# Kernel optimization log

Measured on AMD Instinct MI355X. Metric: run time of the kernel, lower is better.

## Reference

```python
import jax, jax.numpy as jnp
import numpy as np

CH = 256
HEADS = 4
RED = 8  # SE reduction on 2*CH channels


def _conv2d(x, w, pad):
    # x: [b,c,h,w], w: [o,i,kh,kw]
    return jax.lax.conv_general_dilated(
        x, w, window_strides=(1, 1), padding=[(pad, pad), (pad, pad)],
        dimension_numbers=('NCHW', 'OIHW', 'NCHW'))


def setup_inputs() -> dict:
    key = jax.random.key(0)
    ks = jax.random.split(key, 12)
    b, c, h, w = 4, CH, 64, 64
    c2 = 2 * c
    s = 0.02
    inp = {
        'color_feat': jax.random.normal(ks[0], (b, c, h, w), jnp.float32),
        'gray_feat': jax.random.normal(ks[1], (b, c, h, w), jnp.float32),
        'Wq': jax.random.normal(ks[2], (c, c), jnp.float32) * s,
        'Wk': jax.random.normal(ks[3], (c, c), jnp.float32) * s,
        'Wv': jax.random.normal(ks[4], (c, c), jnp.float32) * s,
        'Wproj': jax.random.normal(ks[5], (c, c), jnp.float32) * s,
        'ca_w1': jax.random.normal(ks[6], (c2 // RED, c2), jnp.float32) * s,
        'ca_w2': jax.random.normal(ks[7], (c2, c2 // RED), jnp.float32) * s,
        'sa_w': jax.random.normal(ks[8], (1, 2, 7, 7), jnp.float32) * s,
        'fuse_w': jax.random.normal(ks[9], (c, c2, 3, 3), jnp.float32) * s,
        'bn_gamma': jnp.ones((c,), jnp.float32),
        'bn_beta': jnp.zeros((c,), jnp.float32),
        'bn_mean': jnp.zeros((c,), jnp.float32),
        'bn_var': jnp.ones((c,), jnp.float32),
    }
    return inp


def reference(color_feat, gray_feat, Wq, Wk, Wv, Wproj, ca_w1, ca_w2,
              sa_w, fuse_w, bn_gamma, bn_beta, bn_mean, bn_var):
    b, c, h, w = color_feat.shape
    nh = HEADS
    d = c // nh
    scale = d ** -0.5

    def heads(x, W):
        # 1x1 conv then split heads: [b,c,h,w] -> [b,nh,hw,d]
        y = jnp.einsum('bchw,oc->bohw', x, W)
        return y.reshape(b, nh, d, h * w).transpose(0, 1, 3, 2)

    q = heads(color_feat, Wq)
    k = heads(gray_feat, Wk)
    v = heads(gray_feat, Wv)

    attn = jax.nn.softmax(jnp.einsum('bnid,bnjd->bnij', q, k) * scale, axis=-1)
    out = jnp.einsum('bnij,bnjd->bnid', attn, v)
    out = out.transpose(0, 1, 3, 2).reshape(b, c, h, w)
    out = jnp.einsum('bchw,oc->bohw', out, Wproj)

    cat = jnp.concatenate([out, gray_feat], axis=1)  # [b,2c,h,w]

    # Channel attention (SE with shared MLP on avg- and max-pooled vectors)
    def mlp(z):
        return jax.nn.relu(z @ ca_w1.T) @ ca_w2.T
    avg = cat.mean(axis=(2, 3))
    mx = cat.max(axis=(2, 3))
    wch = jax.nn.sigmoid(mlp(avg) + mlp(mx))[:, :, None, None]
    cat = cat * wch

    # Spatial attention: channel-mean/max -> 7x7 conv -> sigmoid gate
    sa_in = jnp.stack([cat.mean(axis=1), cat.max(axis=1)], axis=1)  # [b,2,h,w]
    wsp = jax.nn.sigmoid(_conv2d(sa_in, sa_w, pad=3))
    cat = cat * wsp

    # Fuse: 3x3 conv -> BatchNorm (inference stats) -> LeakyReLU(0.2)
    y = _conv2d(cat, fuse_w, pad=1)
    inv = bn_gamma / jnp.sqrt(bn_var + 1e-5)
    y = (y - bn_mean[None, :, None, None]) * inv[None, :, None, None] + bn_beta[None, :, None, None]
    return jnp.where(y > 0, y, 0.2 * y)
```

## Files before the change

kernel.cpp:

```cpp
#include <hip/hip_runtime.h>
#include <hip/hip_bf16.h>
#include <stdint.h>

#define HW_ 4096

typedef short bf16x8 __attribute__((ext_vector_type(8)));
typedef short short4v __attribute__((ext_vector_type(4)));
typedef short short8v __attribute__((ext_vector_type(8)));
typedef float f32x4 __attribute__((ext_vector_type(4)));
typedef float f32x16 __attribute__((ext_vector_type(16)));
typedef uint32_t u32x4 __attribute__((ext_vector_type(4)));

__device__ inline unsigned short f2bf(float x) {
  uint32_t u = __builtin_bit_cast(uint32_t, x);
  uint32_t r = ((u >> 16) & 1u) + 0x7fffu;
  return (unsigned short)((u + r) >> 16);
}
__device__ inline uint32_t cvt_pk_bf16(float lo, float hi) {
  uint32_t r;
  asm("v_cvt_pk_bf16_f32 %0, %1, %2" : "=v"(r) : "v"(lo), "v"(hi));
  return r;
}
__device__ inline float bf_lo(uint32_t u) { return __builtin_bit_cast(float, u << 16); }
__device__ inline float bf_hi(uint32_t u) { return __builtin_bit_cast(float, u & 0xffff0000u); }
__device__ inline void gld_lds16(const unsigned short* g, unsigned short* l) {
  __builtin_amdgcn_global_load_lds((const __attribute__((address_space(1))) void*)g,
                                   (__attribute__((address_space(3))) void*)l, 16, 0, 0);
}

#define WAIT_BARRIER(VMSTR)                                                  \
  asm volatile("s_waitcnt " VMSTR "\n\ts_barrier" ::: "memory");             \
  __builtin_amdgcn_sched_barrier(0);

__global__ __launch_bounds__(256) void prep_kernel(
    const float* __restrict__ color, const float* __restrict__ gray,
    const float* __restrict__ Wq, const float* __restrict__ Wk,
    const float* __restrict__ Wv, const float* __restrict__ Wp,
    const float* __restrict__ fw,
    unsigned short* __restrict__ Cbf, unsigned short* __restrict__ Gbf,
    unsigned short* __restrict__ WqB, unsigned short* __restrict__ WkB,
    unsigned short* __restrict__ WvB, unsigned short* __restrict__ WpB,
    unsigned short* __restrict__ wt) {
  const int blk = blockIdx.x;
  const int t = threadIdx.x;
  if (blk < 4096) {
    const float* X = (blk < 2048) ? color : gray;
    unsigned short* Y = (blk < 2048) ? Cbf : Gbf;
    const int i = (blk & 2047) * 256 + t;
    const int p = i & 4095;
    const int cg = (i >> 12) & 31;
    const int b = i >> 17;
    const float* src = X + ((size_t)b * 256 + cg * 8) * HW_ + p;
    float v[8];
#pragma unroll
    for (int e = 0; e < 8; ++e) v[e] = src[(size_t)e * HW_];
    uint4 o;
    o.x = cvt_pk_bf16(v[0], v[1]);
    o.y = cvt_pk_bf16(v[2], v[3]);
    o.z = cvt_pk_bf16(v[4], v[5]);
    o.w = cvt_pk_bf16(v[6], v[7]);
    *(uint4*)&Y[((size_t)(b * 32 + cg) * HW_ + p) * 8] = o;
  } else if (blk < 4224) {
    const int bb = blk - 4096;
    const int which = bb >> 5;
    const float* W = which == 0 ? Wq : which == 1 ? Wk : which == 2 ? Wv : Wp;
    unsigned short* Y = which == 0 ? WqB : which == 1 ? WkB : which == 2 ? WvB : WpB;
    const int i = (bb & 31) * 256 + t;
    const int o = i & 255;
    const int cg = i >> 8;
    float4 a = *(const float4*)&W[(size_t)o * 256 + cg * 8];
    float4 bq = *(const float4*)&W[(size_t)o * 256 + cg * 8 + 4];
    uint4 ov;
    ov.x = cvt_pk_bf16(a.x, a.y);
    ov.y = cvt_pk_bf16(a.z, a.w);
    ov.z = cvt_pk_bf16(bq.x, bq.y);
    ov.w = cvt_pk_bf16(bq.z, bq.w);
    *(uint4*)&Y[((size_t)cg * 256 + o) * 8] = ov;
  } else {
    const size_t i = (size_t)(blk - 4224) * 256 + t;
    const int oc = (int)(i >> 9);
    const int ic = (int)(i & 511);
    const float* src = fw + i * 9;
#pragma unroll
    for (int tap = 0; tap < 9; ++tap)
      wt[((size_t)tap * 256 + oc) * 512 + ic] = f2bf(src[tap]);
  }
}

#define GSTAGE(KS, BUF)                                                       \
  gld_lds16(Xb + ((size_t)((KS) * 2 + (t >> 7)) * HW_ + p0 + (t & 127)) * 8,  \
            &X_l[BUF][0][0][0] + (size_t)t * 8);
#define GCOMP(KS)                                                             \
  {                                                                           \
    bf16x8 af = *(const bf16x8*)&W_l[(KS) * 2 + g32][wo * 32 + n][0];         \
    bf16x8 b0 = *(const bf16x8*)&X_l[(KS) & 3][g32][wp * 64 + n][0];          \
    bf16x8 b1 = *(const bf16x8*)&X_l[(KS) & 3][g32][wp * 64 + 32 + n][0];     \
    acc[0] = __builtin_amdgcn_mfma_f32_32x32x16_bf16(af, b0, acc[0], 0, 0, 0);\
    acc[1] = __builtin_amdgcn_mfma_f32_32x32x16_bf16(af, b1, acc[1], 0, 0, 0);\
  }

__global__ __launch_bounds__(256) void gemm_mfma_kernel(
    const unsigned short* __restrict__ Xbf, const unsigned short* __restrict__ Wbf,
    void* __restrict__ Yv, int mode, float oscale) {
  __shared__ unsigned short W_l[32][64][8];
  __shared__ unsigned short X_l[4][2][128][8];
  const int t = threadIdx.x;
  const int w = t >> 6;
  const int l = t & 63;
  const int n = l & 31;
  const int g32 = l >> 5;
  const int p0 = blockIdx.x * 128;
  const int o0 = blockIdx.y * 64;
  const int b = blockIdx.z;
  const int wo = w >> 1, wp = w & 1;
  const unsigned short* Xb = Xbf + (size_t)b * 32 * HW_ * 8;

#pragma unroll
  for (int j = 0; j < 8; ++j) {
    const int i = j * 256 + t;
    gld_lds16(Wbf + ((size_t)(i >> 6) * 256 + o0 + (i & 63)) * 8,
              &W_l[0][0][0] + (size_t)i * 8);
  }
  GSTAGE(0, 0)
  GSTAGE(1, 1)
  GSTAGE(2, 2)

  f32x16 acc[2] = {};
  for (int ks = 0; ks < 13; ++ks) {
    WAIT_BARRIER("vmcnt(2)")
    GSTAGE(ks + 3, (ks + 3) & 3)
    GCOMP(ks)
  }
  WAIT_BARRIER("vmcnt(2)")
  GCOMP(13)
  WAIT_BARRIER("vmcnt(1)")
  GCOMP(14)
  WAIT_BARRIER("vmcnt(0)")
  GCOMP(15)

  if (mode == 1) {
    unsigned short* Y = (unsigned short*)Yv;
    const size_t bh = (size_t)b * 4 + blockIdx.y;
#pragma unroll
    for (int pf = 0; pf < 2; ++pf) {
      const int p = p0 + wp * 64 + pf * 32 + n;
      unsigned short* dst = Y + (bh * HW_ + p) * 64 + wo * 32 + 4 * g32;
#pragma unroll
      for (int q = 0; q < 4; ++q) {
        uint2 uu;
        uu.x = cvt_pk_bf16(acc[pf][q * 4 + 0] * oscale, acc[pf][q * 4 + 1] * oscale);
        uu.y = cvt_pk_bf16(acc[pf][q * 4 + 2] * oscale, acc[pf][q * 4 + 3] * oscale);
        *(uint2*)&dst[8 * q] = uu;
      }
    }
  } else {
    unsigned short* Y = (unsigned short*)Yv;
    const int cgb = (o0 + wo * 32) >> 3;
#pragma unroll
    for (int pf = 0; pf < 2; ++pf) {
      const int p = p0 + wp * 64 + pf * 32 + n;
#pragma unroll
      for (int q = 0; q < 4; ++q) {
        uint2 uu;
        uu.x = cvt_pk_bf16(acc[pf][q * 4 + 0], acc[pf][q * 4 + 1]);
        uu.y = cvt_pk_bf16(acc[pf][q * 4 + 2], acc[pf][q * 4 + 3]);
        *(uint2*)&Y[((size_t)(b * 32 + cgb + q) * HW_ + p) * 8 + 4 * g32] = uu;
      }
    }
  }
}

#define GCOMP_KV(KS)                                                          \
  {                                                                           \
    bf16x8 afk = *(const bf16x8*)&W_l[0][(KS) * 2 + g32][wo * 32 + n][0];     \
    bf16x8 afv = *(const bf16x8*)&W_l[1][(KS) * 2 + g32][wo * 32 + n][0];     \
    bf16x8 b0 = *(const bf16x8*)&X_l[(KS) & 3][g32][wp * 64 + n][0];          \
    bf16x8 b1 = *(const bf16x8*)&X_l[(KS) & 3][g32][wp * 64 + 32 + n][0];     \
    accK[0] = __builtin_amdgcn_mfma_f32_32x32x16_bf16(afk, b0, accK[0], 0, 0, 0); \
    accK[1] = __builtin_amdgcn_mfma_f32_32x32x16_bf16(afk, b1, accK[1], 0, 0, 0); \
    accV[0] = __builtin_amdgcn_mfma_f32_32x32x16_bf16(afv, b0, accV[0], 0, 0, 0); \
    accV[1] = __builtin_amdgcn_mfma_f32_32x32x16_bf16(afv, b1, accV[1], 0, 0, 0); \
  }

__global__ __launch_bounds__(256) void gemm_kv_kernel(
    const unsigned short* __restrict__ Xbf, const unsigned short* __restrict__ WkB,
    const unsigned short* __restrict__ WvB, unsigned short* __restrict__ Kout,
    unsigned short* __restrict__ Vout) {
  __shared__ unsigned short W_l[2][32][64][8];
  __shared__ unsigned short X_l[4][2][128][8];
  const int t = threadIdx.x;
  const int w = t >> 6;
  const int l = t & 63;
  const int n = l & 31;
  const int g32 = l >> 5;
  const int p0 = blockIdx.x * 128;
  const int o0 = blockIdx.y * 64;
  const int b = blockIdx.z;
  const int wo = w >> 1, wp = w & 1;
  const unsigned short* Xb = Xbf + (size_t)b * 32 * HW_ * 8;

#pragma unroll
  for (int j = 0; j < 16; ++j) {
    const int i = j * 256 + t;
    const int ii = i & 2047;
    const unsigned short* Wsrc = (i >> 11) ? WvB : WkB;
    gld_lds16(Wsrc + ((size_t)(ii >> 6) * 256 + o0 + (ii & 63)) * 8,
              &W_l[0][0][0][0] + (size_t)i * 8);
  }
  GSTAGE(0, 0)
  GSTAGE(1, 1)
  GSTAGE(2, 2)

  f32x16 accK[2] = {};
  f32x16 accV[2] = {};
  for (int ks = 0; ks < 13; ++ks) {
    WAIT_BARRIER("vmcnt(2)")
    GSTAGE(ks + 3, (ks + 3) & 3)
    GCOMP_KV(ks)
  }
  WAIT_BARRIER("vmcnt(2)")
  GCOMP_KV(13)
  WAIT_BARRIER("vmcnt(1)")
  GCOMP_KV(14)
  WAIT_BARRIER("vmcnt(0)")
  GCOMP_KV(15)

  const size_t bh = (size_t)b * 4 + blockIdx.y;
#pragma unroll
  for (int pf = 0; pf < 2; ++pf) {
    const int p = p0 + wp * 64 + pf * 32 + n;
    unsigned short* dst = Kout + (bh * HW_ + p) * 64 + wo * 32 + 4 * g32;
#pragma unroll
    for (int q = 0; q < 4; ++q) {
      uint2 uu;
      uu.x = cvt_pk_bf16(accK[pf][q * 4 + 0], accK[pf][q * 4 + 1]);
      uu.y = cvt_pk_bf16(accK[pf][q * 4 + 2], accK[pf][q * 4 + 3]);
      *(uint2*)&dst[8 * q] = uu;
    }
  }
#pragma unroll
  for (int pf = 0; pf < 2; ++pf) {
    const int p = p0 + wp * 64 + pf * 32 + n;
#pragma unroll
    for (int r = 0; r < 16; ++r) {
      const int m = (r & 3) + 8 * (r >> 2) + 4 * g32;
      Vout[((size_t)b * 256 + o0 + wo * 32 + m) * HW_ + p] = f2bf(accV[pf][r]);
    }
  }
}

#define ATTN_STAGE(SB)                                                       \
  {                                                                          \
    gld_lds16(gKp, kst + (SB) * 4096);                                       \
    gld_lds16(gVp, vst + (SB) * 4096);                                       \
    gKp += 4096;                                                             \
    gVp += 64;                                                               \
  }

#define ATTN_COMPUTE(BUF)                                                    \
  {                                                                          \
    f32x16 aS0 = zero16, aS1 = zero16;                                       \
    __builtin_amdgcn_s_setprio(1);                                           \
    _Pragma("unroll") for (int s = 0; s < 4; ++s) {                          \
      bf16x8 kf0 = *(const bf16x8*)&k_l[(BUF) * 4096 + rowKA + kox[s]];      \
      bf16x8 kf1 = *(const bf16x8*)&k_l[(BUF) * 4096 + rowKB + kox[s]];      \
      aS0 = __builtin_amdgcn_mfma_f32_32x32x16_bf16(kf0, qf[s], aS0, 0, 0, 0); \
      aS1 = __builtin_amdgcn_mfma_f32_32x32x16_bf16(kf1, qf[s], aS1, 0, 0, 0); \
    }                                                                        \
    __builtin_amdgcn_s_setprio(0);                                           \
    float ex0[16], ex1[16];                                                  \
    _Pragma("unroll") for (int r = 0; r < 16; ++r) {                         \
      ex0[r] = __builtin_amdgcn_exp2f(aS0[r]);                               \
      ex1[r] = __builtin_amdgcn_exp2f(aS1[r]);                               \
    }                                                                        \
    float rsp0 = 0.f, rsp1 = 0.f, rsp2 = 0.f, rsp3 = 0.f;                    \
    _Pragma("unroll") for (int r = 0; r < 16; r += 4) {                      \
      rsp0 += ex0[r + 0] + ex1[r + 0];                                       \
      rsp1 += ex0[r + 1] + ex1[r + 1];                                       \
      rsp2 += ex0[r + 2] + ex1[r + 2];                                       \
      rsp3 += ex0[r + 3] + ex1[r + 3];                                       \
    }                                                                        \
    l_r += (rsp0 + rsp1) + (rsp2 + rsp3);                                    \
    union { u32x4 u4; bf16x8 v8; } pA, pB, pC, pD;                           \
    pA.u4 = (u32x4){cvt_pk_bf16(ex0[0], ex0[1]), cvt_pk_bf16(ex0[2], ex0[3]),    \
                    cvt_pk_bf16(ex0[4], ex0[5]), cvt_pk_bf16(ex0[6], ex0[7])};   \
    pB.u4 = (u32x4){cvt_pk_bf16(ex0[8], ex0[9]), cvt_pk_bf16(ex0[10], ex0[11]),  \
                    cvt_pk_bf16(ex0[12], ex0[13]), cvt_pk_bf16(ex0[14], ex0[15])};\
    pC.u4 = (u32x4){cvt_pk_bf16(ex1[0], ex1[1]), cvt_pk_bf16(ex1[2], ex1[3]),    \
                    cvt_pk_bf16(ex1[4], ex1[5]), cvt_pk_bf16(ex1[6], ex1[7])};   \
    pD.u4 = (u32x4){cvt_pk_bf16(ex1[8], ex1[9]), cvt_pk_bf16(ex1[10], ex1[11]),  \
                    cvt_pk_bf16(ex1[12], ex1[13]), cvt_pk_bf16(ex1[14], ex1[15])};\
    __builtin_amdgcn_s_setprio(1);                                           \
    _Pragma("unroll") for (int dh = 0; dh < 2; ++dh) {                       \
      const int rw = (BUF) * 4096 + (dh * 32 + n) * 64;                      \
      union { short4v h2[2]; bf16x8 v8; } v0, v1, v2, v3;                    \
      v0.h2[0] = *(const short4v*)&v_l[rw + voA0];                           \
      v0.h2[1] = *(const short4v*)&v_l[rw + voA1];                           \
      v1.h2[0] = *(const short4v*)&v_l[rw + voB0];                           \
      v1.h2[1] = *(const short4v*)&v_l[rw + voB1];                           \
      v2.h2[0] = *(const short4v*)&v_l[rw + voC0];                           \
      v2.h2[1] = *(const short4v*)&v_l[rw + voC1];                           \
      v3.h2[0] = *(const short4v*)&v_l[rw + voD0];                           \
      v3.h2[1] = *(const short4v*)&v_l[rw + voD1];                           \
      f32x16 ac = accO[dh];                                                  \
      ac = __builtin_amdgcn_mfma_f32_32x32x16_bf16(v0.v8, pA.v8, ac, 0, 0, 0); \
      ac = __builtin_amdgcn_mfma_f32_32x32x16_bf16(v1.v8, pB.v8, ac, 0, 0, 0); \
      ac = __builtin_amdgcn_mfma_f32_32x32x16_bf16(v2.v8, pC.v8, ac, 0, 0, 0); \
      ac = __builtin_amdgcn_mfma_f32_32x32x16_bf16(v3.v8, pD.v8, ac, 0, 0, 0); \
      accO[dh] = ac;                                                         \
    }                                                                        \
    __builtin_amdgcn_s_setprio(0);                                           \
  }

#define ATTN_PHASE(B, SB, VMSTR, DOST)                                       \
  WAIT_BARRIER(VMSTR)                                                        \
  if (DOST) { ATTN_STAGE(SB) }                                               \
  ATTN_COMPUTE(B)

__global__ __launch_bounds__(512) void attn_mfma_kernel(
    const unsigned short* __restrict__ Qb, const unsigned short* __restrict__ Kb,
    const unsigned short* __restrict__ Vb, unsigned short* __restrict__ Abf) {
  __shared__ unsigned short k_l[4 * 4096];
  __shared__ unsigned short v_l[4 * 4096];
  const int t = threadIdx.x;
  const int w = t >> 6;
  const int l = t & 63;
  const int n = l & 31;
  const int h = l >> 5;
  const int bid = blockIdx.x;
  const int gidx = (bid & 7) * 32 + (bid >> 3);
  const int bn = gidx >> 4;
  const int q0 = (gidx & 15) * 256 + w * 32;

  bf16x8 qf[4];
#pragma unroll
  for (int s = 0; s < 4; ++s)
    qf[s] = *(const bf16x8*)&Qb[((size_t)bn * HW_ + q0 + n) * 64 + s * 16 + h * 8];

  const int n7 = n & 7;
  const int rowKA = n * 64;
  const int rowKB = (32 + n) * 64;
  int kox[4];
#pragma unroll
  for (int s = 0; s < 4; ++s) kox[s] = ((2 * s + h) ^ n7) * 8;
  const int h4 = 4 * h;
  const int voA0 = ((0 ^ n7) * 8) + h4, voA1 = ((1 ^ n7) * 8) + h4;
  const int voB0 = ((2 ^ n7) * 8) + h4, voB1 = ((3 ^ n7) * 8) + h4;
  const int voC0 = ((4 ^ n7) * 8) + h4, voC1 = ((5 ^ n7) * 8) + h4;
  const int voD0 = ((6 ^ n7) * 8) + h4, voD1 = ((7 ^ n7) * 8) + h4;

  const int srow = t >> 3;
  const int schunk = (t & 7) ^ (srow & 7);
  const unsigned short* gKp = Kb + ((size_t)bn * HW_ + srow) * 64 + schunk * 8;
  const unsigned short* gVp = Vb + ((size_t)bn * 64 + srow) * HW_ + schunk * 8;
  unsigned short* kst = k_l + w * 512;
  unsigned short* vst = v_l + w * 512;

  f32x16 accO[2] = {};
  float l_r = 0.f;
  const f32x16 zero16 = {};

  ATTN_STAGE(0)
  ATTN_STAGE(1)

  for (int t4 = 0; t4 < 15; ++t4) {
    ATTN_PHASE(0, 2, "vmcnt(2)", 1)
    ATTN_PHASE(1, 3, "vmcnt(2)", 1)
    ATTN_PHASE(2, 0, "vmcnt(2)", 1)
    ATTN_PHASE(3, 1, "vmcnt(2)", 1)
  }
  ATTN_PHASE(0, 2, "vmcnt(2)", 1)
  ATTN_PHASE(1, 3, "vmcnt(2)", 1)
  ATTN_PHASE(2, 0, "vmcnt(2)", 0)
  ATTN_PHASE(3, 0, "vmcnt(0)", 0)

  const int head = bn & 3;
  const int bb = bn >> 2;
  const float lsum = l_r + __shfl_xor(l_r, 32);
  const float inv = 1.0f / lsum;
  const int pcol = q0 + n;
#pragma unroll
  for (int dh = 0; dh < 2; ++dh)
#pragma unroll
    for (int k4 = 0; k4 < 4; ++k4) {
      uint2 uu;
      uu.x = cvt_pk_bf16(accO[dh][k4 * 4 + 0] * inv, accO[dh][k4 * 4 + 1] * inv);
      uu.y = cvt_pk_bf16(accO[dh][k4 * 4 + 2] * inv, accO[dh][k4 * 4 + 3] * inv);
      const int cg = head * 8 + dh * 4 + k4;
      *(uint2*)&Abf[((size_t)(bb * 32 + cg) * HW_ + pcol) * 8 + h4] = uu;
    }
}

__global__ __launch_bounds__(256) void pool_kernel(
    const unsigned short* __restrict__ Pbf, const unsigned short* __restrict__ Gbf,
    float* __restrict__ psum, float* __restrict__ pmaxH) {
  const int cg = blockIdx.x;
  const int b = blockIdx.y;
  const int half = blockIdx.z;
  const int t = threadIdx.x;
  const unsigned short* P = Pbf + ((size_t)(b * 32 + cg) * HW_ + half * 2048) * 8;
  const unsigned short* G = Gbf + ((size_t)(b * 32 + cg) * HW_ + half * 2048) * 8;
  float s[16], m[16];
#pragma unroll
  for (int i = 0; i < 16; ++i) { s[i] = 0.f; m[i] = -1e30f; }
  for (int p = t; p < 2048; p += 256) {
    uint4 a = *(const uint4*)&P[(size_t)p * 8];
    uint4 gg = *(const uint4*)&G[(size_t)p * 8];
    const uint32_t ua[4] = {a.x, a.y, a.z, a.w};
    const uint32_t ug[4] = {gg.x, gg.y, gg.z, gg.w};
#pragma unroll
    for (int q = 0; q < 4; ++q) {
      const float a0 = bf_lo(ua[q]), a1 = bf_hi(ua[q]);
      const float g0 = bf_lo(ug[q]), g1 = bf_hi(ug[q]);
      s[q * 2] += a0; s[q * 2 + 1] += a1;
      m[q * 2] = fmaxf(m[q * 2], a0); m[q * 2 + 1] = fmaxf(m[q * 2 + 1], a1);
      s[8 + q * 2] += g0; s[8 + q * 2 + 1] += g1;
      m[8 + q * 2] = fmaxf(m[8 + q * 2], g0); m[8 + q * 2 + 1] = fmaxf(m[8 + q * 2 + 1], g1);
    }
  }
#pragma unroll
  for (int i = 0; i < 16; ++i)
#pragma unroll
    for (int off = 1; off < 64; off <<= 1) {
      s[i] += __shfl_xor(s[i], off);
      m[i] = fmaxf(m[i], __shfl_xor(m[i], off));
    }
  __shared__ float red[4][32];
  const int wv = t >> 6;
  if ((t & 63) == 0) {
#pragma unroll
    for (int i = 0; i < 16; ++i) { red[wv][i] = s[i]; red[wv][16 + i] = m[i]; }
  }
  __syncthreads();
  if (t < 32) {
    const float v0 = red[0][t], v1 = red[1][t], v2 = red[2][t], v3 = red[3][t];
    if (t < 16) {
      const int ch = (t < 8) ? cg * 8 + t : 256 + cg * 8 + (t - 8);
      psum[half * 2048 + b * 512 + ch] = v0 + v1 + v2 + v3;
    } else {
      const int i = t - 16;
      const int ch = (i < 8) ? cg * 8 + i : 256 + cg * 8 + (i - 8);
      pmaxH[half * 2048 + b * 512 + ch] = fmaxf(fmaxf(v0, v1), fmaxf(v2, v3));
    }
  }
}

__global__ __launch_bounds__(256) void se_kernel(
    const float* __restrict__ psum, const float* __restrict__ pmaxH,
    const float* __restrict__ w1, const float* __restrict__ w2,
    float* __restrict__ wch) {
  const int b = blockIdx.x;
  const int t = threadIdx.x;
  __shared__ float za[512], zm[512], hs[64];
  za[t] = (psum[b * 512 + t] + psum[2048 + b * 512 + t]) * (1.f / 4096.f);
  za[256 + t] = (psum[b * 512 + 256 + t] + psum[2048 + b * 512 + 256 + t]) * (1.f / 4096.f);
  zm[t] = fmaxf(pmaxH[b * 512 + t], pmaxH[2048 + b * 512 + t]);
  zm[256 + t] = fmaxf(pmaxH[b * 512 + 256 + t], pmaxH[2048 + b * 512 + 256 + t]);
  __syncthreads();
  if (t < 64) {
    float ha = 0.f, hm = 0.f;
    for (int c = 0; c < 512; ++c) {
      const float w = w1[t * 512 + c];
      ha += w * za[c];
      hm += w * zm[c];
    }
    hs[t] = fmaxf(ha, 0.f) + fmaxf(hm, 0.f);
  }
  __syncthreads();
  for (int o = t; o < 512; o += 256) {
    float acc = 0.f;
#pragma unroll
    for (int hh = 0; hh < 64; ++hh) acc += hs[hh] * w2[o * 64 + hh];
    wch[b * 512 + o] = 1.f / (1.f + __expf(-acc));
  }
}

__global__ __launch_bounds__(256) void sa_reduce_kernel(
    const unsigned short* __restrict__ Pbf, const unsigned short* __restrict__ Gbf,
    const float* __restrict__ wch, float* __restrict__ sa_in) {
  const int b = blockIdx.y;
  const int t = threadIdx.x;
  const int px = t & 63;
  const int sl = t >> 6;
  const int p = blockIdx.x * 64 + px;
  __shared__ float wl[512];
  __shared__ float sred[4][64], mred[4][64];
  wl[t] = wch[b * 512 + t];
  wl[256 + t] = wch[b * 512 + 256 + t];
  __syncthreads();
  float s = 0.f, mx = -1e30f;
#pragma unroll 4
  for (int k = 0; k < 16; ++k) {
    const int chunk = sl * 16 + k;
    const unsigned short* src = (chunk < 32)
        ? &Pbf[((size_t)(b * 32 + chunk) * HW_ + p) * 8]
        : &Gbf[((size_t)(b * 32 + (chunk - 32)) * HW_ + p) * 8];
    uint4 a = *(const uint4*)src;
    const uint32_t u[4] = {a.x, a.y, a.z, a.w};
#pragma unroll
    for (int q = 0; q < 4; ++q) {
      const float v0 = bf_lo(u[q]) * wl[chunk * 8 + q * 2];
      const float v1 = bf_hi(u[q]) * wl[chunk * 8 + q * 2 + 1];
      s += v0 + v1;
      mx = fmaxf(mx, fmaxf(v0, v1));
    }
  }
  sred[sl][px] = s;
  mred[sl][px] = mx;
  __syncthreads();
  if (sl == 0) {
    const float S = sred[0][px] + sred[1][px] + sred[2][px] + sred[3][px];
    const float M = fmaxf(fmaxf(mred[0][px], mred[1][px]), fmaxf(mred[2][px], mred[3][px]));
    sa_in[((size_t)b * 2 + 0) * HW_ + p] = S * (1.f / 512.f);
    sa_in[((size_t)b * 2 + 1) * HW_ + p] = M;
  }
}

__global__ __launch_bounds__(256) void sa_conv_kernel(
    const float* __restrict__ sa_in, const float* __restrict__ sa_w,
    float* __restrict__ wsp) {
  const int b = blockIdx.y;
  const int t = threadIdx.x;
  __shared__ float pl[2][64][64];
  __shared__ float wl[98];
  for (int e = t; e < 8192; e += 256) ((float*)pl)[e] = sa_in[(size_t)b * 8192 + e];
  if (t < 98) wl[t] = sa_w[t];
  __syncthreads();
  const int pix = blockIdx.x * 256 + t;
  const int y = pix >> 6, x = pix & 63;
  float acc = 0.f;
#pragma unroll
  for (int ic = 0; ic < 2; ++ic)
#pragma unroll
    for (int ky = 0; ky < 7; ++ky) {
      const int yy = y + ky - 3;
      if (yy < 0 || yy > 63) continue;
#pragma unroll
      for (int kx = 0; kx < 7; ++kx) {
        const int xx = x + kx - 3;
        if (xx < 0 || xx > 63) continue;
        acc += pl[ic][yy][xx] * wl[ic * 49 + ky * 7 + kx];
      }
    }
  wsp[(size_t)b * HW_ + pix] = 1.f / (1.f + __expf(-acc));
}

__global__ __launch_bounds__(256) void gate_kernel(
    const unsigned short* __restrict__ Pbf, const unsigned short* __restrict__ Gbf,
    const float* __restrict__ wch, const float* __restrict__ wsp,
    unsigned short* __restrict__ catg) {
  const int yp = blockIdx.x;
  const int xh = blockIdx.y;
  const int b = blockIdx.z;
  const int t = threadIdx.x;
  unsigned short* rowp = catg + ((size_t)b * 66 + yp) * 80 * 512;
  if (yp == 0 || yp == 65) {
    short8v z = {};
    for (int m = t; m < 2560; m += 256)
      *(short8v*)&rowp[((size_t)xh * 40 * 512) + m * 8] = z;
    return;
  }
  const int y = yp - 1;
  __shared__ unsigned short tile[32][512];
  __shared__ float wchl[512];
  __shared__ float wspl[32];
  for (int e = t; e < 512; e += 256) wchl[e] = wch[b * 512 + e];
  if (t < 32) wspl[t] = wsp[(size_t)b * HW_ + y * 64 + xh * 32 + t];
  {
    short8v z = {};
    const int xbase = xh ? 72 : 0;
    for (int m = t; m < 512; m += 256)
      *(short8v*)&rowp[(size_t)(xbase + (m >> 6)) * 512 + (m & 63) * 8] = z;
  }
  __syncthreads();
  const int xl = t & 31;
  const int x = xh * 32 + xl;
  const int cs = t >> 5;
  const float wx = wspl[xl];
#pragma unroll
  for (int k = 0; k < 8; ++k) {
    const int chunk = cs * 8 + k;
    const unsigned short* src = (chunk < 32)
        ? &Pbf[((size_t)(b * 32 + chunk) * HW_ + y * 64 + x) * 8]
        : &Gbf[((size_t)(b * 32 + (chunk - 32)) * HW_ + y * 64 + x) * 8];
    uint4 a = *(const uint4*)src;
    const uint32_t u[4] = {a.x, a.y, a.z, a.w};
    uint32_t o[4];
#pragma unroll
    for (int q = 0; q < 4; ++q) {
      const float lo = bf_lo(u[q]) * wchl[chunk * 8 + q * 2] * wx;
      const float hi = bf_hi(u[q]) * wchl[chunk * 8 + q * 2 + 1] * wx;
      o[q] = cvt_pk_bf16(lo, hi);
    }
    uint4 ov = {o[0], o[1], o[2], o[3]};
    *(uint4*)&tile[xl][(chunk ^ (xl & 7)) * 8] = ov;
  }
  __syncthreads();
#pragma unroll
  for (int j = 0; j < 8; ++j) {
    const int idx = j * 256 + t;
    const int xi_l = idx >> 6;
    const int c8 = idx & 63;
    uint4 v = *(const uint4*)&tile[xi_l][(c8 ^ (xi_l & 7)) * 8];
    *(uint4*)&rowp[(size_t)(xh * 32 + xi_l + 8) * 512 + c8 * 8] = v;
  }
}

__global__ __launch_bounds__(256) void fuse_mfma_kernel(
    const unsigned short* __restrict__ catg, const unsigned short* __restrict__ wt,
    const float* __restrict__ bn_g, const float* __restrict__ bn_b,
    const float* __restrict__ bn_m, const float* __restrict__ bn_v,
    float* __restrict__ out) {
  __shared__ unsigned short X_l[3][6][2][80][8];
  __shared__ unsigned short W_l[3][9][2][32][8];
  __shared__ float invl[32], shl[32];
  const int t = threadIdx.x;
  const int w = t >> 6;
  const int l = t & 63;
  const int n = l & 31;
  const int g = l >> 5;
  const int i = blockIdx.x;
  const int xcd = i & 7, slot = i >> 3;
  const int ocB = slot & 7;
  const int yb = xcd + 8 * (slot >> 3);
  const int y0 = (yb & 15) * 4;
  const int o0 = ocB * 32;
  const int b = yb >> 4;

  if (t < 32) {
    const float iv = bn_g[o0 + t] * rsqrtf(bn_v[o0 + t] + 1e-5f);
    invl[t] = iv;
    shl[t] = bn_b[o0 + t] - bn_m[o0 + t] * iv;
  }

  const unsigned short* catb = catg + ((size_t)b * 66 + y0) * 80 * 512;

  auto stage = [&](int bi, int ic0) {
    for (int wc = w; wc < 16; wc += 4) {
      const int wcc = wc > 14 ? 14 : wc;
      const int m = wcc * 64 + l;
      const int lr = m / 160;
      const int rem = m - lr * 160;
      const int half = rem / 80;
      const int xi = rem - half * 80;
      gld_lds16(catb + ((size_t)lr * 80 + xi) * 512 + ic0 + half * 8,
                &X_l[bi][0][0][0][0] + (size_t)wcc * 512);
    }
    for (int wc = w; wc < 12; wc += 4) {
      const int wcc = wc > 8 ? 8 : wc;
      const int m = wcc * 64 + l;
      const int tap = m >> 6;
      const int rem = m & 63;
      const int half = rem >> 5;
      const int oc = rem & 31;
      gld_lds16(wt + ((size_t)tap * 256 + o0 + oc) * 512 + ic0 + half * 8,
                &W_l[bi][0][0][0][0] + (size_t)wcc * 512);
    }
  };

#define FUSE_COMP(BI)                                                        \
  {                                                                          \
    __builtin_amdgcn_s_setprio(1);                                           \
    _Pragma("unroll") for (int ky = 0; ky < 3; ++ky) {                       \
      const int lr = w + ky;                                                 \
      _Pragma("unroll") for (int kx = 0; kx < 3; ++kx) {                     \
        const int tap = ky * 3 + kx;                                         \
        bf16x8 a0 = *(const bf16x8*)&W_l[BI][tap][g][n][0];                  \
        bf16x8 b0 = *(const bf16x8*)&X_l[BI][lr][g][n + kx + 7][0];          \
        bf16x8 b1 = *(const bf16x8*)&X_l[BI][lr][g][32 + n + kx + 7][0];     \
        acc[0] = __builtin_amdgcn_mfma_f32_32x32x16_bf16(a0, b0, acc[0], 0, 0, 0); \
        acc[1] = __builtin_amdgcn_mfma_f32_32x32x16_bf16(a0, b1, acc[1], 0, 0, 0); \
      }                                                                      \
    }                                                                        \
    __builtin_amdgcn_s_setprio(0);                                           \
  }

  f32x16 acc[2] = {};
  stage(0, 0);
  stage(1, 16);
  for (int kb = 0; kb < 10; ++kb) {
    const int ks = kb * 3;
    WAIT_BARRIER("vmcnt(7)")
    stage(2, (ks + 2) * 16);
    FUSE_COMP(0)
    WAIT_BARRIER("vmcnt(7)")
    stage(0, (ks + 3) * 16);
    FUSE_COMP(1)
    WAIT_BARRIER("vmcnt(7)")
    stage(1, (ks + 4) * 16);
    FUSE_COMP(2)
  }
  WAIT_BARRIER("vmcnt(7)")
  FUSE_COMP(0)
  WAIT_BARRIER("vmcnt(0)")
  FUSE_COMP(1)

#pragma unroll
  for (int pf = 0; pf < 2; ++pf)
#pragma unroll
    for (int r = 0; r < 16; ++r) {
      const int row = (r & 3) + 8 * (r >> 2) + 4 * g;
      const float yv = acc[pf][r] * invl[row] + shl[row];
      const float ov = yv > 0.f ? yv : 0.2f * yv;
      out[((size_t)b * 256 + o0 + row) * HW_ + (size_t)(y0 + w) * 64 + pf * 32 + n] = ov;
    }
}

extern "C" void kernel_launch(void* const* d_in, const int* in_sizes, int n_in,
                              void* d_out, int out_size, void* d_ws, size_t ws_size,
                              hipStream_t stream) {
  const float* color  = (const float*)d_in[0];
  const float* gray   = (const float*)d_in[1];
  const float* Wq     = (const float*)d_in[2];
  const float* Wk     = (const float*)d_in[3];
  const float* Wv     = (const float*)d_in[4];
  const float* Wproj  = (const float*)d_in[5];
  const float* ca_w1  = (const float*)d_in[6];
  const float* ca_w2  = (const float*)d_in[7];
  const float* sa_w   = (const float*)d_in[8];
  const float* fuse_w = (const float*)d_in[9];
  const float* bn_g   = (const float*)d_in[10];
  const float* bn_b   = (const float*)d_in[11];
  const float* bn_m   = (const float*)d_in[12];
  const float* bn_v   = (const float*)d_in[13];
  float* out = (float*)d_out;

  char* ws = (char*)d_ws;
  unsigned short* Cbf = (unsigned short*)(ws);
  unsigned short* Gbf = (unsigned short*)(ws + (8u << 20));
  unsigned short* Qbf = (unsigned short*)(ws + (16u << 20));
  unsigned short* Kbf = (unsigned short*)(ws + (24u << 20));
  unsigned short* Vbf = (unsigned short*)(ws + (32u << 20));
  unsigned short* Abf = (unsigned short*)(ws);
  unsigned short* Pbf = (unsigned short*)(ws + (16u << 20));
  unsigned short* catg = (unsigned short*)(ws + (24u << 20));
  unsigned short* WqB = (unsigned short*)(ws + (45u << 20));
  unsigned short* WkB = WqB + 65536;
  unsigned short* WvB = WkB + 65536;
  unsigned short* WpB = WvB + 65536;
  unsigned short* Wt  = (unsigned short*)(ws + (45u << 20) + (1u << 19));
  float* psum  = (float*)(ws + (48u << 20));
  float* pmaxH = psum + 4096;
  float* wch   = pmaxH + 4096;
  float* sa_in = wch + 2048;
  float* wsp   = sa_in + 32768;
  (void)in_sizes; (void)n_in; (void)out_size; (void)ws_size;

  const float qscale = 0.125f * 1.44269504f;

  prep_kernel<<<dim3(4736), 256, 0, stream>>>(color, gray, Wq, Wk, Wv, Wproj, fuse_w,
                                              Cbf, Gbf, WqB, WkB, WvB, WpB, Wt);

  dim3 g_gemm(32, 4, 4);
  gemm_mfma_kernel<<<g_gemm, 256, 0, stream>>>(Cbf, WqB, Qbf, 1, qscale);
  gemm_kv_kernel<<<g_gemm, 256, 0, stream>>>(Gbf, WkB, WvB, Kbf, Vbf);
  attn_mfma_kernel<<<dim3(256), 512, 0, stream>>>(Qbf, Kbf, Vbf, Abf);
  gemm_mfma_kernel<<<g_gemm, 256, 0, stream>>>(Abf, WpB, Pbf, 3, 1.0f);

  pool_kernel<<<dim3(32, 4, 2), 256, 0, stream>>>(Pbf, Gbf, psum, pmaxH);
  se_kernel<<<dim3(4), 256, 0, stream>>>(psum, pmaxH, ca_w1, ca_w2, wch);
  sa_reduce_kernel<<<dim3(64, 4), 256, 0, stream>>>(Pbf, Gbf, wch, sa_in);
  sa_conv_kernel<<<dim3(16, 4), 256, 0, stream>>>(sa_in, sa_w, wsp);
  gate_kernel<<<dim3(66, 2, 4), 256, 0, stream>>>(Pbf, Gbf, wch, wsp, catg);
  fuse_mfma_kernel<<<dim3(512), 256, 0, stream>>>(catg, Wt, bn_g, bn_b, bn_m, bn_v, out);
}
```

Before: 242.9 us.

## Split attention KV range in two and merge partial outputs in a combine kernel

The attention kernel now splits the key/value sequence into two halves, doubling the grid from 256 to 512 blocks. Each block writes unnormalized bf16 partial outputs plus per-row softmax denominators. A new combine kernel sums the two partials, normalizes them and writes the head-interleaved layout the projection GEMM expects. The goal is more concurrent blocks per CU, and so better latency hiding. In exchange it adds an extra launch, extra workspace traffic and rounding from storing unnormalized partials in bf16.

```diff
diff --git a/kernel.cpp b/kernel.cpp
--- a/kernel.cpp
+++ b/kernel.cpp
@@ -319,7 +319,8 @@
 
 __global__ __launch_bounds__(512) void attn_mfma_kernel(
     const unsigned short* __restrict__ Qb, const unsigned short* __restrict__ Kb,
-    const unsigned short* __restrict__ Vb, unsigned short* __restrict__ Abf) {
+    const unsigned short* __restrict__ Vb, unsigned short* __restrict__ Op0,
+    unsigned short* __restrict__ Op1, float* __restrict__ lpart) {
   __shared__ unsigned short k_l[4 * 4096];
   __shared__ unsigned short v_l[4 * 4096];
   const int t = threadIdx.x;
@@ -328,8 +329,9 @@
   const int n = l & 31;
   const int h = l >> 5;
   const int bid = blockIdx.x;
-  const int gidx = (bid & 7) * 32 + (bid >> 3);
-  const int bn = gidx >> 4;
+  const int gidx = (bid & 7) * 64 + (bid >> 3);
+  const int bn = gidx >> 5;
+  const int split = (gidx >> 4) & 1;
   const int q0 = (gidx & 15) * 256 + w * 32;
 
   bf16x8 qf[4];
@@ -351,8 +353,8 @@
 
   const int srow = t >> 3;
   const int schunk = (t & 7) ^ (srow & 7);
-  const unsigned short* gKp = Kb + ((size_t)bn * HW_ + srow) * 64 + schunk * 8;
-  const unsigned short* gVp = Vb + ((size_t)bn * 64 + srow) * HW_ + schunk * 8;
+  const unsigned short* gKp = Kb + ((size_t)bn * HW_ + split * 2048 + srow) * 64 + schunk * 8;
+  const unsigned short* gVp = Vb + ((size_t)bn * 64 + srow) * HW_ + split * 2048 + schunk * 8;
   unsigned short* kst = k_l + w * 512;
   unsigned short* vst = v_l + w * 512;
 
@@ -363,7 +365,7 @@
   ATTN_STAGE(0)
   ATTN_STAGE(1)
 
-  for (int t4 = 0; t4 < 15; ++t4) {
+  for (int t4 = 0; t4 < 7; ++t4) {
     ATTN_PHASE(0, 2, "vmcnt(2)", 1)
     ATTN_PHASE(1, 3, "vmcnt(2)", 1)
     ATTN_PHASE(2, 0, "vmcnt(2)", 1)
@@ -374,21 +376,46 @@
   ATTN_PHASE(2, 0, "vmcnt(2)", 0)
   ATTN_PHASE(3, 0, "vmcnt(0)", 0)
 
-  const int head = bn & 3;
-  const int bb = bn >> 2;
-  const float lsum = l_r + __shfl_xor(l_r, 32);
-  const float inv = 1.0f / lsum;
+  unsigned short* Op = split ? Op1 : Op0;
   const int pcol = q0 + n;
+  const float ls = l_r + __shfl_xor(l_r, 32);
+  if (h == 0) lpart[((size_t)(split * 16 + bn)) * HW_ + pcol] = ls;
 #pragma unroll
   for (int dh = 0; dh < 2; ++dh)
 #pragma unroll
     for (int k4 = 0; k4 < 4; ++k4) {
       uint2 uu;
-      uu.x = cvt_pk_bf16(accO[dh][k4 * 4 + 0] * inv, accO[dh][k4 * 4 + 1] * inv);
-      uu.y = cvt_pk_bf16(accO[dh][k4 * 4 + 2] * inv, accO[dh][k4 * 4 + 3] * inv);
-      const int cg = head * 8 + dh * 4 + k4;
-      *(uint2*)&Abf[((size_t)(bb * 32 + cg) * HW_ + pcol) * 8 + h4] = uu;
-    }
+      uu.x = cvt_pk_bf16(accO[dh][k4 * 4 + 0], accO[dh][k4 * 4 + 1]);
+      uu.y = cvt_pk_bf16(accO[dh][k4 * 4 + 2], accO[dh][k4 * 4 + 3]);
+      *(uint2*)&Op[((size_t)bn * HW_ + pcol) * 64 + (dh * 4 + k4) * 8 + h4] = uu;
+    }
+}
+
+__global__ __launch_bounds__(256) void attn_combine_kernel(
+    const unsigned short* __restrict__ Op0, const unsigned short* __restrict__ Op1,
+    const float* __restrict__ lpart, unsigned short* __restrict__ Abf) {
+  const int tg = blockIdx.x * 256 + threadIdx.x;
+  const int dg = tg & 7;
+  const int q = (tg >> 3) & 4095;
+  const int bn = tg >> 15;
+  const size_t oidx = ((size_t)bn * HW_ + q) * 64 + dg * 8;
+  uint4 a = *(const uint4*)&Op0[oidx];
+  uint4 b2 = *(const uint4*)&Op1[oidx];
+  const float lsum = lpart[(size_t)bn * HW_ + q] + lpart[(size_t)(16 + bn) * HW_ + q];
+  const float inv = 1.0f / lsum;
+  const uint32_t ua[4] = {a.x, a.y, a.z, a.w};
+  const uint32_t ub[4] = {b2.x, b2.y, b2.z, b2.w};
+  uint32_t o[4];
+#pragma unroll
+  for (int k = 0; k < 4; ++k) {
+    const float lo = (bf_lo(ua[k]) + bf_lo(ub[k])) * inv;
+    const float hi = (bf_hi(ua[k]) + bf_hi(ub[k])) * inv;
+    o[k] = cvt_pk_bf16(lo, hi);
+  }
+  const int head = bn & 3, bb = bn >> 2;
+  const int cg = head * 8 + dg;
+  uint4 ov = {o[0], o[1], o[2], o[3]};
+  *(uint4*)&Abf[((size_t)(bb * 32 + cg) * HW_ + q) * 8] = ov;
 }
 
 __global__ __launch_bounds__(256) void pool_kernel(
@@ -731,15 +758,18 @@
   unsigned short* Qbf = (unsigned short*)(ws + (16u << 20));
   unsigned short* Kbf = (unsigned short*)(ws + (24u << 20));
   unsigned short* Vbf = (unsigned short*)(ws + (32u << 20));
-  unsigned short* Abf = (unsigned short*)(ws);
-  unsigned short* Pbf = (unsigned short*)(ws + (16u << 20));
+  unsigned short* Op0 = (unsigned short*)(ws);
+  unsigned short* Op1 = (unsigned short*)(ws + (48u << 20));
+  float* lpart        = (float*)(ws + (56u << 20));
+  unsigned short* Abf = (unsigned short*)(ws + (16u << 20));
+  unsigned short* Pbf = (unsigned short*)(ws);
   unsigned short* catg = (unsigned short*)(ws + (24u << 20));
   unsigned short* WqB = (unsigned short*)(ws + (45u << 20));
   unsigned short* WkB = WqB + 65536;
   unsigned short* WvB = WkB + 65536;
   unsigned short* WpB = WvB + 65536;
   unsigned short* Wt  = (unsigned short*)(ws + (45u << 20) + (1u << 19));
-  float* psum  = (float*)(ws + (48u << 20));
+  float* psum  = (float*)(ws + (57u << 20));
   float* pmaxH = psum + 4096;
   float* wch   = pmaxH + 4096;
   float* sa_in = wch + 2048;
@@ -754,7 +784,8 @@
   dim3 g_gemm(32, 4, 4);
   gemm_mfma_kernel<<<g_gemm, 256, 0, stream>>>(Cbf, WqB, Qbf, 1, qscale);
   gemm_kv_kernel<<<g_gemm, 256, 0, stream>>>(Gbf, WkB, WvB, Kbf, Vbf);
-  attn_mfma_kernel<<<dim3(256), 512, 0, stream>>>(Qbf, Kbf, Vbf, Abf);
+  attn_mfma_kernel<<<dim3(512), 512, 0, stream>>>(Qbf, Kbf, Vbf, Op0, Op1, lpart);
+  attn_combine_kernel<<<dim3(2048), 256, 0, stream>>>(Op0, Op1, lpart, Abf);
   gemm_mfma_kernel<<<g_gemm, 256, 0, stream>>>(Abf, WpB, Pbf, 3, 1.0f);
 
   pool_kernel<<<dim3(32, 4, 2), 256, 0, stream>>>(Pbf, Gbf, psum, pmaxH);
```

Measured after the change: 254.3 us. 1.05x slower.
